# Performance work log

Hardware: AMD Instinct MI355X
Metric: run time of the kernel (lower is better)

## Reference

```python
import jax, jax.numpy as jnp
import numpy as np

NUM_NODES = 262144        # 1024 graphs x 256 nodes
NODES_PER_GRAPH = 256
NUM_GRAPHS = NUM_NODES // NODES_PER_GRAPH
NUM_EDGES = 2097152       # avg degree 8
NUM_FEATURES = 9
NUM_STATIONS = 8


def setup_inputs() -> dict:
    key = jax.random.key(0)
    ks = jax.random.split(key, 12)
    # edges constrained within each graph so batched-graph semantics hold
    src_local = jax.random.randint(ks[0], (NUM_EDGES,), 0, NODES_PER_GRAPH)
    dst_local = jax.random.randint(ks[1], (NUM_EDGES,), 0, NODES_PER_GRAPH)
    graph_of_edge = jax.random.randint(ks[2], (NUM_EDGES,), 0, NUM_GRAPHS)
    offset = graph_of_edge * NODES_PER_GRAPH
    edge_index = jnp.stack([src_local + offset, dst_local + offset]).astype(jnp.int64)
    station_ids = jnp.array([0, 37, 73, 110, 146, 183, 219, 255], dtype=jnp.int64)
    s = lambda k, shape, fan_in: jax.random.normal(k, shape, jnp.float32) / np.sqrt(fan_in)
    return {
        "x": jax.random.normal(ks[3], (NUM_NODES, NUM_FEATURES), jnp.float32),
        "edge_index": edge_index,
        "station_ids": station_ids,
        "W1": s(ks[4], (NUM_FEATURES, 32), NUM_FEATURES),
        "b1": jnp.zeros((32,), jnp.float32),
        "W2": s(ks[5], (32, 64), 32),
        "b2": jnp.zeros((64,), jnp.float32),
        "fc1_W": s(ks[6], (128, 64), 128),
        "fc1_b": jnp.zeros((64,), jnp.float32),
        "fc2_W": s(ks[7], (64, 1), 64),
        "fc2_b": jnp.zeros((1,), jnp.float32),
    }


def _gcn_conv(x, W, b, src, dst, n_nodes):
    """PyG GCNConv: add self-loops, symmetric normalization, linear first."""
    h = x @ W                                              # [N, C_out]
    # degree includes the self-loop (+1), counted on target nodes
    deg = jnp.zeros((n_nodes,), h.dtype).at[dst].add(1.0) + 1.0
    dinv = jax.lax.rsqrt(deg)                              # deg >= 1, safe
    norm = dinv[src] * dinv[dst]                           # [E]
    out = jnp.zeros_like(h).at[dst].add(norm[:, None] * h[src])
    out = out + (dinv * dinv)[:, None] * h                 # self-loop term
    return out + b


def reference(x, edge_index, station_ids, W1, b1, W2, b2, fc1_W, fc1_b, fc2_W, fc2_b):
    n = x.shape[0]
    src, dst = edge_index[0], edge_index[1]
    h = jax.nn.relu(_gcn_conv(x, W1, b1, src, dst, n))     # [N, 32]
    h = jax.nn.relu(_gcn_conv(h, W2, b2, src, dst, n))     # [N, 64]
    # global mean pool per graph (batch = node_idx // NODES_PER_GRAPH)
    batch = jnp.arange(n) // NODES_PER_GRAPH
    sums = jax.ops.segment_sum(h, batch, num_segments=NUM_GRAPHS)
    counts = jax.ops.segment_sum(jnp.ones((n,), h.dtype), batch, num_segments=NUM_GRAPHS)
    global_ctx = sums / counts[:, None]                    # [B, 64]
    # per-station gather-MLP, vectorized over stations
    idx = jnp.arange(NUM_GRAPHS)[:, None] * NODES_PER_GRAPH + station_ids[None, :]  # [B, S]
    station_emb = h[idx]                                   # [B, S, 64]
    ctx = jnp.broadcast_to(global_ctx[:, None, :], station_emb.shape)
    combined = jnp.concatenate([station_emb, ctx], axis=-1)  # [B, S, 128]
    q = jax.nn.relu(combined @ fc1_W + fc1_b) @ fc2_W + fc2_b  # [B, S, 1]
    return q[..., 0]                                       # [B, S]
```

## Files before the change

### kernel.cpp

```cpp
#include <hip/hip_runtime.h>
#include <hip/hip_bf16.h>


#define NNODES 262144
#define NPG 256
#define NGRAPHS 1024
#define NEDGES 2097152
#define NFEAT 9
#define ECAP2 2560
#define T_EDGES 8192
#define NTILES (NEDGES / T_EDGES)
#define TPB 512
#define NBLK 256

typedef __hip_bfloat16 bf16;
typedef short short8 __attribute__((ext_vector_type(8)));
typedef float f32x4 __attribute__((ext_vector_type(4)));

__device__ __forceinline__ float bfbits(unsigned short u) { return __uint_as_float(((unsigned)u) << 16); }
__device__ __forceinline__ unsigned short f2bbits(float v) { bf16 b = __float2bfloat16(v); return *(unsigned short*)&b; }


__global__ void __launch_bounds__(1024) k_hist(const int* __restrict__ dst,
                                               int* __restrict__ hist) {
    __shared__ int cnt[NGRAPHS];
    int t = threadIdx.x;
    cnt[t] = 0;
    __syncthreads();
    const int4* d4 = (const int4*)(dst + blockIdx.x * T_EDGES);
#pragma unroll
    for (int k = 0; k < T_EDGES / 4096; ++k) {
        int4 dv = d4[k * 1024 + t];
        atomicAdd(&cnt[dv.x >> 8], 1);
        atomicAdd(&cnt[dv.y >> 8], 1);
        atomicAdd(&cnt[dv.z >> 8], 1);
        atomicAdd(&cnt[dv.w >> 8], 1);
    }
    __syncthreads();
    hist[blockIdx.x * NGRAPHS + t] = cnt[t];
}

__global__ void __launch_bounds__(256) k_scan(int* __restrict__ hist,
                                              int* __restrict__ gcnt) {
    __shared__ int wsum[4];
    int g = blockIdx.x;
    int t = threadIdx.x;
    int lane = t & 63, wv = t >> 6;
    int v = hist[t * NGRAPHS + g];
    int inc = v;
    for (int off = 1; off < 64; off <<= 1) {
        int y = __shfl_up(inc, off);
        if (lane >= off) inc += y;
    }
    if (lane == 63) wsum[wv] = inc;
    __syncthreads();
    int wpre = 0;
#pragma unroll
    for (int w = 0; w < 3; ++w) if (w < wv) wpre += wsum[w];
    int exc = wpre + inc - v;
    hist[t * NGRAPHS + g] = exc;
    if (t == 255) gcnt[g * 16] = exc + v;
}

__global__ void __launch_bounds__(1024) k_scatter(const int* __restrict__ src,
                                                  const int* __restrict__ dst,
                                                  const int* __restrict__ hist,
                                                  unsigned short* __restrict__ gout) {
    __shared__ unsigned short sg[T_EDGES];
    __shared__ unsigned short pay[T_EDGES];
    __shared__ unsigned short spay[T_EDGES];
    __shared__ unsigned short ssg[T_EDGES];
    __shared__ int cnt[NGRAPHS];
    __shared__ int lbase[NGRAPHS];
    __shared__ int gb[NGRAPHS];
    __shared__ int wsum[16];
    int t = threadIdx.x;
    int lane = t & 63, wv = t >> 6;
    int base = blockIdx.x * T_EDGES;
    cnt[t] = 0;
    gb[t] = hist[blockIdx.x * NGRAPHS + t];
    __syncthreads();
    const int4* s4 = (const int4*)(src + base);
    const int4* d4 = (const int4*)(dst + base);
#pragma unroll
    for (int k = 0; k < T_EDGES / 4096; ++k) {
        int idx = k * 1024 + t;
        int4 dv = d4[idx];
        int4 sv = s4[idx];
        int i0 = idx * 4;
        sg[i0]     = (unsigned short)(dv.x >> 8);
        sg[i0 + 1] = (unsigned short)(dv.y >> 8);
        sg[i0 + 2] = (unsigned short)(dv.z >> 8);
        sg[i0 + 3] = (unsigned short)(dv.w >> 8);
        pay[i0]     = (unsigned short)(((dv.x & 255) << 8) | (sv.x & 255));
        pay[i0 + 1] = (unsigned short)(((dv.y & 255) << 8) | (sv.y & 255));
        pay[i0 + 2] = (unsigned short)(((dv.z & 255) << 8) | (sv.z & 255));
        pay[i0 + 3] = (unsigned short)(((dv.w & 255) << 8) | (sv.w & 255));
        atomicAdd(&cnt[dv.x >> 8], 1);
        atomicAdd(&cnt[dv.y >> 8], 1);
        atomicAdd(&cnt[dv.z >> 8], 1);
        atomicAdd(&cnt[dv.w >> 8], 1);
    }
    __syncthreads();
    int c = cnt[t];
    int inc = c;
    for (int off = 1; off < 64; off <<= 1) {
        int y = __shfl_up(inc, off);
        if (lane >= off) inc += y;
    }
    if (lane == 63) wsum[wv] = inc;
    __syncthreads();
    int wpre = 0;
    for (int w = 0; w < wv; ++w) wpre += wsum[w];
    lbase[t] = wpre + inc - c;
    cnt[t] = 0;
    __syncthreads();
#pragma unroll
    for (int k = 0; k < T_EDGES / 1024; ++k) {
        int i = k * 1024 + t;
        int g = sg[i];
        int p = lbase[g] + atomicAdd(&cnt[g], 1);
        spay[p] = pay[i];
        ssg[p] = (unsigned short)g;
    }
    __syncthreads();
#pragma unroll
    for (int k = 0; k < T_EDGES / 1024; ++k) {
        int p = k * 1024 + t;
        int g = ssg[p];
        int off = gb[g] + (p - lbase[g]);
        if (off < ECAP2) gout[(size_t)g * ECAP2 + off] = spay[p];
    }
}


__global__ void __launch_bounds__(TPB) k_fused(
    const float* __restrict__ x, const int* __restrict__ station_ids,
    const float* __restrict__ W1, const float* __restrict__ b1,
    const float* __restrict__ W2, const float* __restrict__ b2,
    const float* __restrict__ fc1W, const float* __restrict__ fc1b,
    const float* __restrict__ fc2W, const float* __restrict__ fc2b,
    const int* __restrict__ gcnt, const unsigned short* __restrict__ gedges,
    float* __restrict__ out) {

    __shared__ __align__(16) unsigned char Ms[65536];
    __shared__ __align__(16) unsigned char BufA[17024];
    __shared__ __align__(16) unsigned char BufB[17024];
    __shared__ __align__(16) unsigned char BufC[19456];
    __shared__ __align__(16) unsigned short fc1s16[8192];
    __shared__ __align__(16) unsigned short W2Ts[64 * 40];
    __shared__ float W1s[288];
    __shared__ float dinvs[256];
    __shared__ unsigned short Rl[260];
    __shared__ unsigned char El[ECAP2];
    __shared__ unsigned int sru[512];
    __shared__ float sts[512];
    __shared__ float meanf[64];
    __shared__ float poolf[64];
    __shared__ unsigned char stmap[256];
    __shared__ float b1s[32], b2s[64], fc1bs[64], fc2ws[64];
    __shared__ int stids[8];
    __shared__ float fc2bv;

    int t = threadIdx.x;
    int lane = t & 63, wvid = t >> 6;
    int m = lane & 15, quad = lane >> 4;

    float* xsf = (float*)BufC;
    unsigned short* EPa = (unsigned short*)(BufC + 9216);
    unsigned short* G1T = (unsigned short*)BufA;
    unsigned short* H1T = (unsigned short*)BufB;
    unsigned short* S2 = (unsigned short*)BufC;

    for (int i = t; i < NFEAT * 32; i += TPB) W1s[i] = W1[i];
    for (int i = t; i < 2048; i += TPB)
        W2Ts[(i >> 5) * 40 + (i & 31)] = f2bbits(W2[(i & 31) * 64 + (i >> 5)]);
    for (int i = t; i < 8192; i += TPB) fc1s16[i] = f2bbits(fc1W[i]);
    if (t < 32) b1s[t] = b1[t];
    if (t < 64) { b2s[t] = b2[t]; fc1bs[t] = fc1b[t]; fc2ws[t] = fc2W[t]; }
    if (t < 8) stids[t] = station_ids[t];
    if (t == 0) fc2bv = fc2b[0];
    if (t < 256) stmap[t] = 255;
    __syncthreads();
    if (t < 8) stmap[stids[t] & 255] = (unsigned char)t;

    for (int g = blockIdx.x; g < NGRAPHS; g += NBLK) {
        int nbase = g * NPG;

        int ecnt = min(gcnt[g * 16], ECAP2);
        {
            const uint4* gev = (const uint4*)(gedges + (size_t)g * ECAP2);
            uint4* epv = (uint4*)EPa;
            for (int i = t; i < ECAP2 / 8; i += TPB) epv[i] = gev[i];
        }
        const float* xg = x + (size_t)nbase * NFEAT;
        for (int i = t; i < NPG * NFEAT; i += TPB) xsf[i] = xg[i];
        if (t < 64) poolf[t] = 0.f;
        if (t < 256) sru[t] = 0u;
        {
            uint4* mz = (uint4*)Ms;
            uint4 z = {0u, 0u, 0u, 0u};
            for (int i = t; i < 4096; i += TPB) mz[i] = z;
        }
        __syncthreads();

        for (int i = t; i < ecnt; i += TPB) atomicAdd(&sru[EPa[i] >> 8], 1u);
        __syncthreads();

        if (wvid == 0) {
            int b0 = sru[lane * 4], b1v = sru[lane * 4 + 1], b2v = sru[lane * 4 + 2], b3 = sru[lane * 4 + 3];
            int s = b0 + b1v + b2v + b3;
            int inc = s;
            for (int off = 1; off < 64; off <<= 1) {
                int y = __shfl_up(inc, off);
                if (lane >= off) inc += y;
            }
            int run = inc - s;
            Rl[lane * 4] = (unsigned short)run; sru[256 + lane * 4] = run;
            dinvs[lane * 4] = rsqrtf((float)(b0 + 1)); run += b0;
            Rl[lane * 4 + 1] = (unsigned short)run; sru[257 + lane * 4] = run;
            dinvs[lane * 4 + 1] = rsqrtf((float)(b1v + 1)); run += b1v;
            Rl[lane * 4 + 2] = (unsigned short)run; sru[258 + lane * 4] = run;
            dinvs[lane * 4 + 2] = rsqrtf((float)(b2v + 1)); run += b2v;
            Rl[lane * 4 + 3] = (unsigned short)run; sru[259 + lane * 4] = run;
            dinvs[lane * 4 + 3] = rsqrtf((float)(b3 + 1));
            if (lane == 63) Rl[256] = (unsigned short)inc;
        }
        __syncthreads();

        for (int i = t; i < ecnt; i += TPB) {
            unsigned short v = EPa[i];
            unsigned p = atomicAdd(&sru[256 + (v >> 8)], 1u);
            if (p < ECAP2) El[p] = (unsigned char)(v & 255);
        }
        __syncthreads();

        if (t < 256) {
            int dl = t >> 1, q = t & 1;
            int d = dl;
            float did = dinvs[d];
            if ((d >> 7) == q)
                *(unsigned short*)(Ms + dl * 512 + (((d >> 3) ^ (d & 15)) * 16) + (d & 7) * 2)
                    = f2bbits(did * did);
            int r0 = Rl[d], r1 = Rl[d + 1];
            for (int e = r0; e < r1; ++e) {
                int s = El[e];
                if ((s >> 7) == q) {
                    unsigned short* p =
                        (unsigned short*)(Ms + dl * 512 + (((s >> 3) ^ (d & 15)) * 16) + (s & 7) * 2);
                    *p = f2bbits(bfbits(*p) + did * dinvs[s]);
                }
            }
        } else {
            int n = t - 256;
            float xv[NFEAT];
#pragma unroll
            for (int k = 0; k < NFEAT; k++) xv[k] = xsf[n * NFEAT + k];
#pragma unroll 4
            for (int c = 0; c < 32; c++) {
                float acc = 0.f;
#pragma unroll
                for (int k = 0; k < NFEAT; k++) acc += xv[k] * W1s[k * 32 + c];
                G1T[c * 266 + n] = f2bbits(acc);
            }
        }
        __syncthreads();

        {
            f32x4 acc[2] = {};
            for (int kt = 0; kt < 8; ++kt) {
                short8 af = *(const short8*)(Ms + (wvid * 16 + m) * 512 + (((kt * 4 + quad) ^ m) * 16));
                short8 bf0 = *(const short8*)(BufA + (size_t)m * 532 + kt * 64 + quad * 16);
                short8 bf1 = *(const short8*)(BufA + (size_t)(16 + m) * 532 + kt * 64 + quad * 16);
                acc[0] = __builtin_amdgcn_mfma_f32_16x16x32_bf16(af, bf0, acc[0], 0, 0, 0);
                acc[1] = __builtin_amdgcn_mfma_f32_16x16x32_bf16(af, bf1, acc[1], 0, 0, 0);
            }
#pragma unroll
            for (int ni = 0; ni < 2; ++ni) {
                int ch = ni * 16 + m;
                float bb = b1s[ch];
#pragma unroll
                for (int r = 0; r < 4; ++r) {
                    int node = wvid * 16 + quad * 4 + r;
                    H1T[ch * 266 + node] = f2bbits(fmaxf(acc[ni][r] + bb, 0.f));
                }
            }
        }
        __syncthreads();

        {
            uint4* mz = (uint4*)Ms;
            uint4 z = {0u, 0u, 0u, 0u};
            for (int i = t; i < 4096; i += TPB) mz[i] = z;
        }
        __syncthreads();
        {
            int dl = t >> 2, q = t & 3;
            int d = 128 + dl;
            float did = dinvs[d];
            if (((d & 255) >> 6) == q) {
                int sd = d & 255;
                *(unsigned short*)(Ms + dl * 512 + (((sd >> 3) ^ (d & 15)) * 16) + (sd & 7) * 2)
                    = f2bbits(did * did);
            }
            int r0 = Rl[d], r1 = Rl[d + 1];
            for (int e = r0; e < r1; ++e) {
                int s = El[e];
                if ((s >> 6) == q) {
                    unsigned short* p =
                        (unsigned short*)(Ms + dl * 512 + (((s >> 3) ^ (d & 15)) * 16) + (s & 7) * 2);
                    *p = f2bbits(bfbits(*p) + did * dinvs[s]);
                }
            }
        }
        __syncthreads();

        {
            f32x4 acc[2] = {};
            for (int kt = 0; kt < 8; ++kt) {
                short8 af = *(const short8*)(Ms + (wvid * 16 + m) * 512 + (((kt * 4 + quad) ^ m) * 16));
                short8 bf0 = *(const short8*)(BufA + (size_t)m * 532 + kt * 64 + quad * 16);
                short8 bf1 = *(const short8*)(BufA + (size_t)(16 + m) * 532 + kt * 64 + quad * 16);
                acc[0] = __builtin_amdgcn_mfma_f32_16x16x32_bf16(af, bf0, acc[0], 0, 0, 0);
                acc[1] = __builtin_amdgcn_mfma_f32_16x16x32_bf16(af, bf1, acc[1], 0, 0, 0);
            }
#pragma unroll
            for (int ni = 0; ni < 2; ++ni) {
                int ch = ni * 16 + m;
                float bb = b1s[ch];
#pragma unroll
                for (int r = 0; r < 4; ++r) {
                    int node = 128 + wvid * 16 + quad * 4 + r;
                    H1T[ch * 266 + node] = f2bbits(fmaxf(acc[ni][r] + bb, 0.f));
                }
            }
        }
        __syncthreads();

        {
            f32x4 acc[2] = {};
            for (int kt = 0; kt < 8; ++kt) {
                short8 af = *(const short8*)(Ms + (wvid * 16 + m) * 512 + (((kt * 4 + quad) ^ m) * 16));
                short8 bf0 = *(const short8*)(BufB + (size_t)m * 532 + kt * 64 + quad * 16);
                short8 bf1 = *(const short8*)(BufB + (size_t)(16 + m) * 532 + kt * 64 + quad * 16);
                acc[0] = __builtin_amdgcn_mfma_f32_16x16x32_bf16(af, bf0, acc[0], 0, 0, 0);
                acc[1] = __builtin_amdgcn_mfma_f32_16x16x32_bf16(af, bf1, acc[1], 0, 0, 0);
            }
#pragma unroll
            for (int ni = 0; ni < 2; ++ni) {
                int ch = ni * 16 + m;
#pragma unroll
                for (int r = 0; r < 4; ++r) {
                    int node = 128 + wvid * 16 + quad * 4 + r;
                    S2[node * 38 + ch] = f2bbits(acc[ni][r]);
                }
            }
        }
        __syncthreads();

        {
            uint4* mz = (uint4*)Ms;
            uint4 z = {0u, 0u, 0u, 0u};
            for (int i = t; i < 4096; i += TPB) mz[i] = z;
        }
        __syncthreads();
        {
            int dl = t >> 2, q = t & 3;
            int d = dl;
            float did = dinvs[d];
            if ((d >> 6) == q)
                *(unsigned short*)(Ms + dl * 512 + (((d >> 3) ^ (d & 15)) * 16) + (d & 7) * 2)
                    = f2bbits(did * did);
            int r0 = Rl[d], r1 = Rl[d + 1];
            for (int e = r0; e < r1; ++e) {
                int s = El[e];
                if ((s >> 6) == q) {
                    unsigned short* p =
                        (unsigned short*)(Ms + dl * 512 + (((s >> 3) ^ (d & 15)) * 16) + (s & 7) * 2);
                    *p = f2bbits(bfbits(*p) + did * dinvs[s]);
                }
            }
        }
        __syncthreads();

        {
            f32x4 acc[2] = {};
            for (int kt = 0; kt < 8; ++kt) {
                short8 af = *(const short8*)(Ms + (wvid * 16 + m) * 512 + (((kt * 4 + quad) ^ m) * 16));
                short8 bf0 = *(const short8*)(BufB + (size_t)m * 532 + kt * 64 + quad * 16);
                short8 bf1 = *(const short8*)(BufB + (size_t)(16 + m) * 532 + kt * 64 + quad * 16);
                acc[0] = __builtin_amdgcn_mfma_f32_16x16x32_bf16(af, bf0, acc[0], 0, 0, 0);
                acc[1] = __builtin_amdgcn_mfma_f32_16x16x32_bf16(af, bf1, acc[1], 0, 0, 0);
            }
#pragma unroll
            for (int ni = 0; ni < 2; ++ni) {
                int ch = ni * 16 + m;
#pragma unroll
                for (int r = 0; r < 4; ++r) {
                    int node = wvid * 16 + quad * 4 + r;
                    S2[node * 38 + ch] = f2bbits(acc[ni][r]);
                }
            }
        }
        __syncthreads();

        {
#pragma unroll
            for (int mi = 0; mi < 2; ++mi) {
                int mt = wvid * 2 + mi;
                short8 af = *(const short8*)(BufC + (size_t)(mt * 16 + m) * 76 + quad * 16);
#pragma unroll
                for (int ni = 0; ni < 4; ++ni) {
                    short8 bf = *(const short8*)((const unsigned char*)W2Ts + (size_t)(ni * 16 + m) * 80 + quad * 16);
                    f32x4 c = {};
                    c = __builtin_amdgcn_mfma_f32_16x16x32_bf16(af, bf, c, 0, 0, 0);
                    int ch = ni * 16 + m;
                    float bb = b2s[ch];
                    float hv[4];
                    float p = 0.f;
#pragma unroll
                    for (int r = 0; r < 4; ++r) { hv[r] = fmaxf(c[r] + bb, 0.f); p += hv[r]; }
                    p += __shfl_down(p, 32);
                    p += __shfl_down(p, 16);
                    if (quad == 0) atomicAdd(&poolf[ch], p);
#pragma unroll
                    for (int r = 0; r < 4; ++r) {
                        int node = mt * 16 + quad * 4 + r;
                        int si = stmap[node];
                        if (si != 255) sts[si * 64 + ch] = hv[r];
                    }
                }
            }
        }
        __syncthreads();

        if (t < 64) meanf[t] = poolf[t] * (1.0f / 256.0f);
        __syncthreads();

        {
            int l = lane;
            int si = wvid;
            const float* st = sts + si * 64;
            float acc = 0.f;
#pragma unroll 8
            for (int k = 0; k < 64; k++) acc += st[k] * bfbits(fc1s16[k * 64 + l]);
#pragma unroll 8
            for (int k = 0; k < 64; k++) acc += meanf[k] * bfbits(fc1s16[(64 + k) * 64 + l]);
            float a = fmaxf(acc + fc1bs[l], 0.f) * fc2ws[l];
            for (int off = 32; off > 0; off >>= 1) a += __shfl_down(a, off);
            if (l == 0) out[g * 8 + si] = a + fc2bv;
        }
        __syncthreads();
    }
}


extern "C" void kernel_launch(void* const* d_in, const int* in_sizes, int n_in,
                              void* d_out, int out_size, void* d_ws, size_t ws_size,
                              hipStream_t stream) {
    const float* x = (const float*)d_in[0];
    const int* ei = (const int*)d_in[1];
    const int* station_ids = (const int*)d_in[2];
    const float* W1 = (const float*)d_in[3];
    const float* b1 = (const float*)d_in[4];
    const float* W2 = (const float*)d_in[5];
    const float* bias2 = (const float*)d_in[6];
    const float* fc1W = (const float*)d_in[7];
    const float* fc1b = (const float*)d_in[8];
    const float* fc2W = (const float*)d_in[9];
    const float* fc2b = (const float*)d_in[10];
    float* out = (float*)d_out;
    (void)in_sizes; (void)n_in; (void)out_size; (void)ws_size;

    char* ws = (char*)d_ws;
    int* gcnt = (int*)ws;
    unsigned short* gout = (unsigned short*)(ws + 0x10000);
    int* hist = (int*)(ws + 0x510000);

    const int* esrc = ei;
    const int* edst = ei + NEDGES;

    k_hist<<<NTILES, 1024, 0, stream>>>(edst, hist);
    k_scan<<<NGRAPHS, 256, 0, stream>>>(hist, gcnt);
    k_scatter<<<NTILES, 1024, 0, stream>>>(esrc, edst, hist, gout);
    k_fused<<<NBLK, TPB, 0, stream>>>(x, station_ids, W1, b1, W2, bias2,
                                      fc1W, fc1b, fc2W, fc2b, gcnt, gout, out);
}
```

Baseline: 191.3 us.

## Double block size to 1024 threads and split MFMA/scatter work across more waves

```diff
diff --git a/kernel.cpp b/kernel.cpp
--- a/kernel.cpp
+++ b/kernel.cpp
@@ -10,7 +10,7 @@
 #define ECAP2 2560
 #define T_EDGES 8192
 #define NTILES (NEDGES / T_EDGES)
-#define TPB 512
+#define TPB 1024
 #define NBLK 256
 
 typedef __hip_bfloat16 bf16;
@@ -165,6 +165,7 @@
     int t = threadIdx.x;
     int lane = t & 63, wvid = t >> 6;
     int m = lane & 15, quad = lane >> 4;
+    int wr = wvid >> 1, wn = wvid & 1;
 
     float* xsf = (float*)BufC;
     unsigned short* EPa = (unsigned short*)(BufC + 9216);
@@ -235,136 +236,7 @@
         }
         __syncthreads();
 
-        if (t < 256) {
-            int dl = t >> 1, q = t & 1;
-            int d = dl;
-            float did = dinvs[d];
-            if ((d >> 7) == q)
-                *(unsigned short*)(Ms + dl * 512 + (((d >> 3) ^ (d & 15)) * 16) + (d & 7) * 2)
-                    = f2bbits(did * did);
-            int r0 = Rl[d], r1 = Rl[d + 1];
-            for (int e = r0; e < r1; ++e) {
-                int s = El[e];
-                if ((s >> 7) == q) {
-                    unsigned short* p =
-                        (unsigned short*)(Ms + dl * 512 + (((s >> 3) ^ (d & 15)) * 16) + (s & 7) * 2);
-                    *p = f2bbits(bfbits(*p) + did * dinvs[s]);
-                }
-            }
-        } else {
-            int n = t - 256;
-            float xv[NFEAT];
-#pragma unroll
-            for (int k = 0; k < NFEAT; k++) xv[k] = xsf[n * NFEAT + k];
-#pragma unroll 4
-            for (int c = 0; c < 32; c++) {
-                float acc = 0.f;
-#pragma unroll
-                for (int k = 0; k < NFEAT; k++) acc += xv[k] * W1s[k * 32 + c];
-                G1T[c * 266 + n] = f2bbits(acc);
-            }
-        }
-        __syncthreads();
-
-        {
-            f32x4 acc[2] = {};
-            for (int kt = 0; kt < 8; ++kt) {
-                short8 af = *(const short8*)(Ms + (wvid * 16 + m) * 512 + (((kt * 4 + quad) ^ m) * 16));
-                short8 bf0 = *(const short8*)(BufA + (size_t)m * 532 + kt * 64 + quad * 16);
-                short8 bf1 = *(const short8*)(BufA + (size_t)(16 + m) * 532 + kt * 64 + quad * 16);
-                acc[0] = __builtin_amdgcn_mfma_f32_16x16x32_bf16(af, bf0, acc[0], 0, 0, 0);
-                acc[1] = __builtin_amdgcn_mfma_f32_16x16x32_bf16(af, bf1, acc[1], 0, 0, 0);
-            }
-#pragma unroll
-            for (int ni = 0; ni < 2; ++ni) {
-                int ch = ni * 16 + m;
-                float bb = b1s[ch];
-#pragma unroll
-                for (int r = 0; r < 4; ++r) {
-                    int node = wvid * 16 + quad * 4 + r;
-                    H1T[ch * 266 + node] = f2bbits(fmaxf(acc[ni][r] + bb, 0.f));
-                }
-            }
-        }
-        __syncthreads();
-
-        {
-            uint4* mz = (uint4*)Ms;
-            uint4 z = {0u, 0u, 0u, 0u};
-            for (int i = t; i < 4096; i += TPB) mz[i] = z;
-        }
-        __syncthreads();
-        {
-            int dl = t >> 2, q = t & 3;
-            int d = 128 + dl;
-            float did = dinvs[d];
-            if (((d & 255) >> 6) == q) {
-                int sd = d & 255;
-                *(unsigned short*)(Ms + dl * 512 + (((sd >> 3) ^ (d & 15)) * 16) + (sd & 7) * 2)
-                    = f2bbits(did * did);
-            }
-            int r0 = Rl[d], r1 = Rl[d + 1];
-            for (int e = r0; e < r1; ++e) {
-                int s = El[e];
-                if ((s >> 6) == q) {
-                    unsigned short* p =
-                        (unsigned short*)(Ms + dl * 512 + (((s >> 3) ^ (d & 15)) * 16) + (s & 7) * 2);
-                    *p = f2bbits(bfbits(*p) + did * dinvs[s]);
-                }
-            }
-        }
-        __syncthreads();
-
-        {
-            f32x4 acc[2] = {};
-            for (int kt = 0; kt < 8; ++kt) {
-                short8 af = *(const short8*)(Ms + (wvid * 16 + m) * 512 + (((kt * 4 + quad) ^ m) * 16));
-                short8 bf0 = *(const short8*)(BufA + (size_t)m * 532 + kt * 64 + quad * 16);
-                short8 bf1 = *(const short8*)(BufA + (size_t)(16 + m) * 532 + kt * 64 + quad * 16);
-                acc[0] = __builtin_amdgcn_mfma_f32_16x16x32_bf16(af, bf0, acc[0], 0, 0, 0);
-                acc[1] = __builtin_amdgcn_mfma_f32_16x16x32_bf16(af, bf1, acc[1], 0, 0, 0);
-            }
-#pragma unroll
-            for (int ni = 0; ni < 2; ++ni) {
-                int ch = ni * 16 + m;
-                float bb = b1s[ch];
-#pragma unroll
-                for (int r = 0; r < 4; ++r) {
-                    int node = 128 + wvid * 16 + quad * 4 + r;
-                    H1T[ch * 266 + node] = f2bbits(fmaxf(acc[ni][r] + bb, 0.f));
-                }
-            }
-        }
-        __syncthreads();
-
-        {
-            f32x4 acc[2] = {};
-            for (int kt = 0; kt < 8; ++kt) {
-                short8 af = *(const short8*)(Ms + (wvid * 16 + m) * 512 + (((kt * 4 + quad) ^ m) * 16));
-                short8 bf0 = *(const short8*)(BufB + (size_t)m * 532 + kt * 64 + quad * 16);
-                short8 bf1 = *(const short8*)(BufB + (size_t)(16 + m) * 532 + kt * 64 + quad * 16);
-                acc[0] = __builtin_amdgcn_mfma_f32_16x16x32_bf16(af, bf0, acc[0], 0, 0, 0);
-                acc[1] = __builtin_amdgcn_mfma_f32_16x16x32_bf16(af, bf1, acc[1], 0, 0, 0);
-            }
-#pragma unroll
-            for (int ni = 0; ni < 2; ++ni) {
-                int ch = ni * 16 + m;
-#pragma unroll
-                for (int r = 0; r < 4; ++r) {
-                    int node = 128 + wvid * 16 + quad * 4 + r;
-                    S2[node * 38 + ch] = f2bbits(acc[ni][r]);
-                }
-            }
-        }
-        __syncthreads();
-
-        {
-            uint4* mz = (uint4*)Ms;
-            uint4 z = {0u, 0u, 0u, 0u};
-            for (int i = t; i < 4096; i += TPB) mz[i] = z;
-        }
-        __syncthreads();
-        {
+        if (t < 512) {
             int dl = t >> 2, q = t & 3;
             int d = dl;
             float did = dinvs[d];
@@ -380,64 +252,173 @@
                     *p = f2bbits(bfbits(*p) + did * dinvs[s]);
                 }
             }
-        }
-        __syncthreads();
-
-        {
-            f32x4 acc[2] = {};
+        } else {
+            int tt = t - 512;
+            int n = tt >> 1, half = tt & 1;
+            float xv[NFEAT];
+#pragma unroll
+            for (int k = 0; k < NFEAT; k++) xv[k] = xsf[n * NFEAT + k];
+            int c0 = half * 16;
+#pragma unroll 4
+            for (int ci = 0; ci < 16; ci++) {
+                int c = c0 + ci;
+                float acc = 0.f;
+#pragma unroll
+                for (int k = 0; k < NFEAT; k++) acc += xv[k] * W1s[k * 32 + c];
+                G1T[c * 266 + n] = f2bbits(acc);
+            }
+        }
+        __syncthreads();
+
+        {
+            f32x4 acc = {};
             for (int kt = 0; kt < 8; ++kt) {
-                short8 af = *(const short8*)(Ms + (wvid * 16 + m) * 512 + (((kt * 4 + quad) ^ m) * 16));
-                short8 bf0 = *(const short8*)(BufB + (size_t)m * 532 + kt * 64 + quad * 16);
-                short8 bf1 = *(const short8*)(BufB + (size_t)(16 + m) * 532 + kt * 64 + quad * 16);
-                acc[0] = __builtin_amdgcn_mfma_f32_16x16x32_bf16(af, bf0, acc[0], 0, 0, 0);
-                acc[1] = __builtin_amdgcn_mfma_f32_16x16x32_bf16(af, bf1, acc[1], 0, 0, 0);
-            }
-#pragma unroll
-            for (int ni = 0; ni < 2; ++ni) {
+                short8 af = *(const short8*)(Ms + (wr * 16 + m) * 512 + (((kt * 4 + quad) ^ m) * 16));
+                short8 bf = *(const short8*)(BufA + (size_t)(wn * 16 + m) * 532 + kt * 64 + quad * 16);
+                acc = __builtin_amdgcn_mfma_f32_16x16x32_bf16(af, bf, acc, 0, 0, 0);
+            }
+            int ch = wn * 16 + m;
+            float bb = b1s[ch];
+#pragma unroll
+            for (int r = 0; r < 4; ++r) {
+                int node = wr * 16 + quad * 4 + r;
+                H1T[ch * 266 + node] = f2bbits(fmaxf(acc[r] + bb, 0.f));
+            }
+        }
+        __syncthreads();
+
+        {
+            uint4* mz = (uint4*)Ms;
+            uint4 z = {0u, 0u, 0u, 0u};
+            for (int i = t; i < 4096; i += TPB) mz[i] = z;
+        }
+        __syncthreads();
+        {
+            int dl = t >> 3, q = t & 7;
+            int d = 128 + dl;
+            float did = dinvs[d];
+            int sd = d & 255;
+            if ((sd >> 5) == q) {
+                *(unsigned short*)(Ms + dl * 512 + (((sd >> 3) ^ (d & 15)) * 16) + (sd & 7) * 2)
+                    = f2bbits(did * did);
+            }
+            int r0 = Rl[d], r1 = Rl[d + 1];
+            for (int e = r0; e < r1; ++e) {
+                int s = El[e];
+                if ((s >> 5) == q) {
+                    unsigned short* p =
+                        (unsigned short*)(Ms + dl * 512 + (((s >> 3) ^ (d & 15)) * 16) + (s & 7) * 2);
+                    *p = f2bbits(bfbits(*p) + did * dinvs[s]);
+                }
+            }
+        }
+        __syncthreads();
+
+        {
+            f32x4 acc = {};
+            for (int kt = 0; kt < 8; ++kt) {
+                short8 af = *(const short8*)(Ms + (wr * 16 + m) * 512 + (((kt * 4 + quad) ^ m) * 16));
+                short8 bf = *(const short8*)(BufA + (size_t)(wn * 16 + m) * 532 + kt * 64 + quad * 16);
+                acc = __builtin_amdgcn_mfma_f32_16x16x32_bf16(af, bf, acc, 0, 0, 0);
+            }
+            int ch = wn * 16 + m;
+            float bb = b1s[ch];
+#pragma unroll
+            for (int r = 0; r < 4; ++r) {
+                int node = 128 + wr * 16 + quad * 4 + r;
+                H1T[ch * 266 + node] = f2bbits(fmaxf(acc[r] + bb, 0.f));
+            }
+        }
+        __syncthreads();
+
+        {
+            f32x4 acc = {};
+            for (int kt = 0; kt < 8; ++kt) {
+                short8 af = *(const short8*)(Ms + (wr * 16 + m) * 512 + (((kt * 4 + quad) ^ m) * 16));
+                short8 bf = *(const short8*)(BufB + (size_t)(wn * 16 + m) * 532 + kt * 64 + quad * 16);
+                acc = __builtin_amdgcn_mfma_f32_16x16x32_bf16(af, bf, acc, 0, 0, 0);
+            }
+            int ch = wn * 16 + m;
+#pragma unroll
+            for (int r = 0; r < 4; ++r) {
+                int node = 128 + wr * 16 + quad * 4 + r;
+                S2[node * 38 + ch] = f2bbits(acc[r]);
+            }
+        }
+        __syncthreads();
+
+        {
+            uint4* mz = (uint4*)Ms;
+            uint4 z = {0u, 0u, 0u, 0u};
+            for (int i = t; i < 4096; i += TPB) mz[i] = z;
+        }
+        __syncthreads();
+        {
+            int dl = t >> 3, q = t & 7;
+            int d = dl;
+            float did = dinvs[d];
+            if ((d >> 5) == q)
+                *(unsigned short*)(Ms + dl * 512 + (((d >> 3) ^ (d & 15)) * 16) + (d & 7) * 2)
+                    = f2bbits(did * did);
+            int r0 = Rl[d], r1 = Rl[d + 1];
+            for (int e = r0; e < r1; ++e) {
+                int s = El[e];
+                if ((s >> 5) == q) {
+                    unsigned short* p =
+                        (unsigned short*)(Ms + dl * 512 + (((s >> 3) ^ (d & 15)) * 16) + (s & 7) * 2);
+                    *p = f2bbits(bfbits(*p) + did * dinvs[s]);
+                }
+            }
+        }
+        __syncthreads();
+
+        {
+            f32x4 acc = {};
+            for (int kt = 0; kt < 8; ++kt) {
+                short8 af = *(const short8*)(Ms + (wr * 16 + m) * 512 + (((kt * 4 + quad) ^ m) * 16));
+                short8 bf = *(const short8*)(BufB + (size_t)(wn * 16 + m) * 532 + kt * 64 + quad * 16);
+                acc = __builtin_amdgcn_mfma_f32_16x16x32_bf16(af, bf, acc, 0, 0, 0);
+            }
+            int ch = wn * 16 + m;
+#pragma unroll
+            for (int r = 0; r < 4; ++r) {
+                int node = wr * 16 + quad * 4 + r;
+                S2[node * 38 + ch] = f2bbits(acc[r]);
+            }
+        }
+        __syncthreads();
+
+        {
+            int mt = wvid;
+            short8 af = *(const short8*)(BufC + (size_t)(mt * 16 + m) * 76 + quad * 16);
+#pragma unroll
+            for (int ni = 0; ni < 4; ++ni) {
+                short8 bf = *(const short8*)((const unsigned char*)W2Ts + (size_t)(ni * 16 + m) * 80 + quad * 16);
+                f32x4 c = {};
+                c = __builtin_amdgcn_mfma_f32_16x16x32_bf16(af, bf, c, 0, 0, 0);
                 int ch = ni * 16 + m;
+                float bb = b2s[ch];
+                float hv[4];
+                float p = 0.f;
+#pragma unroll
+                for (int r = 0; r < 4; ++r) { hv[r] = fmaxf(c[r] + bb, 0.f); p += hv[r]; }
+                p += __shfl_down(p, 32);
+                p += __shfl_down(p, 16);
+                if (quad == 0) atomicAdd(&poolf[ch], p);
 #pragma unroll
                 for (int r = 0; r < 4; ++r) {
-                    int node = wvid * 16 + quad * 4 + r;
-                    S2[node * 38 + ch] = f2bbits(acc[ni][r]);
+                    int node = mt * 16 + quad * 4 + r;
+                    int si = stmap[node];
+                    if (si != 255) sts[si * 64 + ch] = hv[r];
                 }
             }
         }
         __syncthreads();
 
-        {
-#pragma unroll
-            for (int mi = 0; mi < 2; ++mi) {
-                int mt = wvid * 2 + mi;
-                short8 af = *(const short8*)(BufC + (size_t)(mt * 16 + m) * 76 + quad * 16);
-#pragma unroll
-                for (int ni = 0; ni < 4; ++ni) {
-                    short8 bf = *(const short8*)((const unsigned char*)W2Ts + (size_t)(ni * 16 + m) * 80 + quad * 16);
-                    f32x4 c = {};
-                    c = __builtin_amdgcn_mfma_f32_16x16x32_bf16(af, bf, c, 0, 0, 0);
-                    int ch = ni * 16 + m;
-                    float bb = b2s[ch];
-                    float hv[4];
-                    float p = 0.f;
-#pragma unroll
-                    for (int r = 0; r < 4; ++r) { hv[r] = fmaxf(c[r] + bb, 0.f); p += hv[r]; }
-                    p += __shfl_down(p, 32);
-                    p += __shfl_down(p, 16);
-                    if (quad == 0) atomicAdd(&poolf[ch], p);
-#pragma unroll
-                    for (int r = 0; r < 4; ++r) {
-                        int node = mt * 16 + quad * 4 + r;
-                        int si = stmap[node];
-                        if (si != 255) sts[si * 64 + ch] = hv[r];
-                    }
-                }
-            }
-        }
-        __syncthreads();
-
         if (t < 64) meanf[t] = poolf[t] * (1.0f / 256.0f);
         __syncthreads();
 
-        {
+        if (wvid < 8) {
             int l = lane;
             int si = wvid;
             const float* st = sts + si * 64;
```

After: 188.0 us. Within noise of the previous version (-1.7%).
